# Kernel optimization log

Measured on AMD Instinct MI355X. Metric: run time of the kernel, lower is better.

## Reference

```python
import jax, jax.numpy as jnp
import numpy as np

D = 1024
H = 16
HD = D // H
EPS = 1e-5

def _ln(t, gamma, beta):
    # LayerNorm over last dim (head_dim)
    mu = jnp.mean(t, axis=-1, keepdims=True)
    var = jnp.mean(jnp.square(t - mu), axis=-1, keepdims=True)
    return (t - mu) * jax.lax.rsqrt(var + EPS) * gamma + beta

def setup_inputs() -> dict:
    key = jax.random.key(0)
    ks = jax.random.split(key, 6)
    B, S = 2, 2048
    # xavier_uniform bound for square [D,D] weight
    bound = float(np.sqrt(6.0 / (D + D)))
    x = jax.random.normal(ks[0], (B, S, D), dtype=jnp.float32)
    Wq = jax.random.uniform(ks[1], (D, D), jnp.float32, -bound, bound)
    Wk = jax.random.uniform(ks[2], (D, D), jnp.float32, -bound, bound)
    Wv = jax.random.uniform(ks[3], (D, D), jnp.float32, -bound, bound)
    Wp = jax.random.uniform(ks[4], (D, D), jnp.float32, -bound, bound)
    bp = jnp.zeros((D,), jnp.float32)
    gq = jnp.ones((HD,), jnp.float32); bq = jnp.zeros((HD,), jnp.float32)
    gk = jnp.ones((HD,), jnp.float32); bk = jnp.zeros((HD,), jnp.float32)
    return {"x": x, "Wq": Wq, "Wk": Wk, "Wv": Wv, "Wp": Wp, "bp": bp,
            "gq": gq, "bq": bq, "gk": gk, "bk": bk}

def reference(x, Wq, Wk, Wv, Wp, bp, gq, bq, gk, bk):
    B, S, _ = x.shape
    scale = HD ** -0.5
    # torch Linear: x @ W.T -> (B,S,H,HD) -> (B,H,S,HD)
    q = (x @ Wq.T).reshape(B, S, H, HD).transpose(0, 2, 1, 3)
    k = (x @ Wk.T).reshape(B, S, H, HD).transpose(0, 2, 1, 3)
    v = (x @ Wv.T).reshape(B, S, H, HD).transpose(0, 2, 1, 3)
    q = _ln(q, gq, bq)
    k = _ln(k, gk, bk)
    scores = jnp.einsum('bhqd,bhkd->bhqk', q, k) * scale
    causal_mask = jnp.triu(jnp.ones((S, S), dtype=bool), k=1)  # True above diagonal
    scores = jnp.where(causal_mask[None, None], -jnp.inf, scores)
    attn = jax.nn.softmax(scores, axis=-1)
    out = jnp.einsum('bhqk,bhkd->bhqd', attn, v).transpose(0, 2, 1, 3).reshape(B, S, D)
    out = out @ Wp.T + bp
    return (out, attn)
```

## Files before the change

### kernel.cpp

```cpp
#include <hip/hip_runtime.h>

typedef _Float16 f16;
typedef _Float16 f16x4 __attribute__((ext_vector_type(4)));
typedef _Float16 f16x8 __attribute__((ext_vector_type(8)));
typedef float f32x4 __attribute__((ext_vector_type(4)));

#define D_ 1024
#define H_ 16
#define HD_ 64
#define B_ 2
#define S_ 2048
#define M_ 4096
#define SCALE 0.125f
#define NEG_BIG -1e30f

__device__ __forceinline__ float red16_sum(float v) {
#pragma unroll
  for (int m = 8; m >= 1; m >>= 1) v += __shfl_xor(v, m);
  return v;
}

__device__ __forceinline__ void gload16(const f16* g, f16* l) {
  __builtin_amdgcn_global_load_lds((const __attribute__((address_space(1))) void*)g,
                                   (__attribute__((address_space(3))) void*)l, 16, 0, 0);
}

__global__ __launch_bounds__(256) void k_cvt5(const float* __restrict__ x,
    const float* __restrict__ w0, const float* __restrict__ w1,
    const float* __restrict__ w2, const float* __restrict__ w3,
    f16* __restrict__ xh, f16* __restrict__ wh)
{
  const int y = blockIdx.y;
  const float* src; f16* dst; int n4;
  if (y == 0) { src = x; dst = xh; n4 = (M_ * D_) / 4; }
  else {
    src = (y == 1) ? w0 : (y == 2) ? w1 : (y == 3) ? w2 : w3;
    dst = wh + (size_t)(y - 1) * D_ * D_;
    n4 = (D_ * D_) / 4;
  }
  const int stride = gridDim.x * blockDim.x;
  for (int i = blockIdx.x * blockDim.x + threadIdx.x; i < n4; i += stride) {
    f32x4 v = ((const f32x4*)src)[i];
    ((f16x4*)dst)[i] = (f16x4){(f16)v[0], (f16)v[1], (f16)v[2], (f16)v[3]};
  }
}

__device__ __forceinline__ void gemm128(const f16* __restrict__ A, const f16* __restrict__ Bw,
                                        int K, int bm, int bn, f32x4 acc[4][4])
{
  __shared__ f16 As[128][64];
  __shared__ f16 Bs[128][64];
  const int tid = threadIdx.x;
  const int lane = tid & 63, wid = tid >> 6;
  const int wr = wid >> 1, wc = wid & 1, g = lane >> 4, li = lane & 15;
  const int lrow = lane >> 3, lcol = (lane & 7) * 8;

#pragma unroll
  for (int m = 0; m < 4; ++m)
#pragma unroll
    for (int n = 0; n < 4; ++n)
      acc[m][n] = (f32x4){0.f, 0.f, 0.f, 0.f};

  for (int k0 = 0; k0 < K; k0 += 64) {
#pragma unroll
    for (int i = 0; i < 4; ++i) {
      int c = wid * 4 + i;
      int row = c * 8 + lrow;
      gload16(&A[(size_t)(bm + row) * K + k0 + lcol], &As[c * 8][0]);
      gload16(&Bw[(size_t)(bn + row) * K + k0 + lcol], &Bs[c * 8][0]);
    }
    __syncthreads();
#pragma unroll
    for (int kk = 0; kk < 64; kk += 32) {
      f16x8 af[4], bf[4];
#pragma unroll
      for (int m = 0; m < 4; ++m) af[m] = *(const f16x8*)&As[wr * 64 + m * 16 + li][kk + g * 8];
#pragma unroll
      for (int n = 0; n < 4; ++n) bf[n] = *(const f16x8*)&Bs[wc * 64 + n * 16 + li][kk + g * 8];
#pragma unroll
      for (int m = 0; m < 4; ++m)
#pragma unroll
        for (int n = 0; n < 4; ++n)
          acc[m][n] = __builtin_amdgcn_mfma_f32_16x16x32_f16(af[m], bf[n], acc[m][n], 0, 0, 0);
    }
    __syncthreads();
  }
}

__global__ __launch_bounds__(256) void k_gemm_qkv(const f16* __restrict__ xh,
    const f16* __restrict__ wh,
    const float* __restrict__ gq, const float* __restrict__ bq,
    const float* __restrict__ gk, const float* __restrict__ bk,
    f16* __restrict__ qt, f16* __restrict__ kt, f16* __restrict__ vh)
{
  const int z = blockIdx.z;
  const f16* Bw = wh + (size_t)z * D_ * D_;
  f16* C = (z == 0) ? qt : (z == 1) ? kt : vh;
  f32x4 acc[4][4];
  gemm128(xh, Bw, D_, blockIdx.x * 128, blockIdx.y * 128, acc);
  const int tid = threadIdx.x, lane = tid & 63, wid = tid >> 6;
  const int wr = wid >> 1, wc = wid & 1, g = lane >> 4, li = lane & 15;
  const int hh = blockIdx.y * 2 + wc;
  const float* gamma = (z == 0) ? gq : gk;
  const float* beta  = (z == 0) ? bq : bk;
  float gm[4], bt[4];
  if (z < 2) {
#pragma unroll
    for (int n = 0; n < 4; ++n) { gm[n] = gamma[n * 16 + li]; bt[n] = beta[n * 16 + li]; }
  }
#pragma unroll
  for (int m = 0; m < 4; ++m)
#pragma unroll
    for (int r = 0; r < 4; ++r) {
      int rr = blockIdx.x * 128 + wr * 64 + m * 16 + g * 4 + r;
      int b = rr >> 11, s = rr & (S_ - 1);
      float v0 = acc[m][0][r], v1 = acc[m][1][r], v2 = acc[m][2][r], v3 = acc[m][3][r];
      if (z < 2) {
        float mean = red16_sum(v0 + v1 + v2 + v3) * (1.f / 64.f);
        v0 -= mean; v1 -= mean; v2 -= mean; v3 -= mean;
        float ss = red16_sum(v0 * v0 + v1 * v1 + v2 * v2 + v3 * v3);
        float inv = rsqrtf(ss * (1.f / 64.f) + 1e-5f);
        v0 = v0 * inv * gm[0] + bt[0]; v1 = v1 * inv * gm[1] + bt[1];
        v2 = v2 * inv * gm[2] + bt[2]; v3 = v3 * inv * gm[3] + bt[3];
      }
      f16* dst = C + ((size_t)(b * H_ + hh) * S_ + s) * HD_;
      dst[li]      = (f16)v0;
      dst[16 + li] = (f16)v1;
      dst[32 + li] = (f16)v2;
      dst[48 + li] = (f16)v3;
    }
}

__global__ __launch_bounds__(256) void k_gemm_proj(const f16* __restrict__ oh,
    const f16* __restrict__ Wph, const float* __restrict__ bp, float* __restrict__ out)
{
  f32x4 acc[4][4];
  gemm128(oh, Wph, D_, blockIdx.x * 128, blockIdx.y * 128, acc);
  const int tid = threadIdx.x, lane = tid & 63, wid = tid >> 6;
  const int wr = wid >> 1, wc = wid & 1, g = lane >> 4, li = lane & 15;
#pragma unroll
  for (int m = 0; m < 4; ++m)
#pragma unroll
    for (int n = 0; n < 4; ++n)
#pragma unroll
      for (int r = 0; r < 4; ++r) {
        int rr = blockIdx.x * 128 + wr * 64 + m * 16 + g * 4 + r;
        int cc = blockIdx.y * 128 + wc * 64 + n * 16 + li;
        out[(size_t)rr * D_ + cc] = acc[m][n][r] + bp[cc];
      }
}

__global__ __launch_bounds__(256) void k_transpose_v(const f16* __restrict__ vh, f16* __restrict__ vt)
{
  __shared__ f16 T[64][72];
  const int tid = threadIdx.x;
  const int s0 = blockIdx.x * 64, h = blockIdx.y, b = blockIdx.z;
  const f16* src = vh + ((size_t)(b * H_ + h) * S_ + s0) * HD_;
#pragma unroll
  for (int i = 0; i < 2; ++i) {
    int slot = tid + i * 256, sl = slot >> 3, ch = (slot & 7) * 8;
    *(f16x8*)&T[sl][ch] = *(const f16x8*)&src[(size_t)sl * HD_ + ch];
  }
  __syncthreads();
#pragma unroll
  for (int i = 0; i < 2; ++i) {
    int slot = tid + i * 256, d = slot >> 3, sc = (slot & 7) * 8;
    f16x8 val;
#pragma unroll
    for (int j = 0; j < 8; ++j) val[j] = T[sc + j][d];
    *(f16x8*)&vt[((size_t)(b * H_ + h) * HD_ + d) * S_ + s0 + sc] = val;
  }
}

__global__ __launch_bounds__(256, 4) void k_attn_stats(const f16* __restrict__ qt,
    const f16* __restrict__ kt, float* __restrict__ lpart)
{
  __shared__ float Ls[2][64];
  const int tq = 31 - blockIdx.x;
  const int ks = blockIdx.y;
  const int bh = blockIdx.z;
  const int tid = threadIdx.x, lane = tid & 63, wid = tid >> 6;
  const int wr = wid >> 1, wc = wid & 1, g = lane >> 4, li = lane & 15;
  const int ntk = (tq + 2) >> 1;
  const int t0 = ks * 8, t1 = (ntk < (ks + 1) * 8) ? ntk : (ks + 1) * 8;
  float* lp = lpart + ((size_t)(bh * 32 + tq) * 2 + ks) * 64;
  if (t0 >= t1) { if (tid < 64) lp[tid] = 0.f; return; }

  const f16* Qb = qt + (size_t)bh * S_ * HD_;
  const f16* Kb = kt + (size_t)bh * S_ * HD_;

  f16x8 qa[2][2];
#pragma unroll
  for (int m = 0; m < 2; ++m)
#pragma unroll
    for (int kk = 0; kk < 2; ++kk)
      qa[m][kk] = *(const f16x8*)&Qb[(size_t)(tq * 64 + wr * 32 + m * 16 + li) * HD_ + kk * 32 + g * 8];

  float lrun[2][4];
#pragma unroll
  for (int m = 0; m < 2; ++m)
#pragma unroll
    for (int r = 0; r < 4; ++r) lrun[m][r] = 0.f;

  for (int tk = t0; tk < t1; ++tk) {
    f32x4 acc[2][4];
#pragma unroll
    for (int m = 0; m < 2; ++m)
#pragma unroll
      for (int n = 0; n < 4; ++n) acc[m][n] = (f32x4){0.f, 0.f, 0.f, 0.f};
#pragma unroll
    for (int kk = 0; kk < 2; ++kk) {
      f16x8 kf[4];
#pragma unroll
      for (int n = 0; n < 4; ++n)
        kf[n] = *(const f16x8*)&Kb[(size_t)(tk * 128 + wc * 64 + n * 16 + li) * HD_ + kk * 32 + g * 8];
#pragma unroll
      for (int m = 0; m < 2; ++m)
#pragma unroll
        for (int n = 0; n < 4; ++n)
          acc[m][n] = __builtin_amdgcn_mfma_f32_16x16x32_f16(qa[m][kk], kf[n], acc[m][n], 0, 0, 0);
    }
    const bool diag = (tk == ntk - 1);
#pragma unroll
    for (int m = 0; m < 2; ++m)
#pragma unroll
      for (int r = 0; r < 4; ++r) {
        int row = tq * 64 + wr * 32 + m * 16 + g * 4 + r;
#pragma unroll
        for (int n = 0; n < 4; ++n) {
          float sv = acc[m][n][r] * SCALE;
          if (diag) { int col = tk * 128 + wc * 64 + n * 16 + li; if (col > row) sv = NEG_BIG; }
          lrun[m][r] += __expf(sv);
        }
      }
  }

#pragma unroll
  for (int m = 0; m < 2; ++m)
#pragma unroll
    for (int r = 0; r < 4; ++r) lrun[m][r] = red16_sum(lrun[m][r]);

  if (li == 0) {
#pragma unroll
    for (int m = 0; m < 2; ++m)
#pragma unroll
      for (int r = 0; r < 4; ++r)
        Ls[wc][wr * 32 + m * 16 + g * 4 + r] = lrun[m][r];
  }
  __syncthreads();
  if (tid < 64) lp[tid] = Ls[0][tid] + Ls[1][tid];
}

__global__ __launch_bounds__(64, 4) void k_attn_fused(const f16* __restrict__ qt,
    const f16* __restrict__ kt, const f16* __restrict__ vt,
    const float* __restrict__ lpart, float* __restrict__ attn, f16* __restrict__ oh)
{
  __shared__ f16 Ps[16][138];
  const int bx = blockIdx.x;
  const int bh = bx & 31;
  const int s  = 127 - (bx >> 5);
  const int b = bh >> 4, h = bh & 15;
  const int lane = threadIdx.x;
  const int g = lane >> 4, li = lane & 15;
  const int row0 = s * 16;
  const int ntk = (s + 8) >> 3;
  const f16* Qb = qt + (size_t)bh * S_ * HD_;
  const f16* Kb = kt + (size_t)bh * S_ * HD_;
  float* attnB = attn + (size_t)bh * S_ * S_;
  const float* lp = lpart + (size_t)(bh * 32 + (s >> 2)) * 2 * 64;

  f16x8 qa[2];
#pragma unroll
  for (int kk = 0; kk < 2; ++kk)
    qa[kk] = *(const f16x8*)&Qb[(size_t)(row0 + li) * HD_ + kk * 32 + g * 8];

  float il[4];
#pragma unroll
  for (int r = 0; r < 4; ++r) {
    int lr = (s & 3) * 16 + g * 4 + r;
    il[r] = 1.f / (lp[lr] + lp[64 + lr]);
  }

  f32x4 oacc[4];
#pragma unroll
  for (int n = 0; n < 4; ++n) oacc[n] = (f32x4){0.f, 0.f, 0.f, 0.f};

  for (int tk = 0; tk < ntk; ++tk) {
    const bool diag = (tk == ntk - 1);
#pragma unroll
    for (int nh = 0; nh < 2; ++nh) {
      f32x4 acc[4];
#pragma unroll
      for (int j = 0; j < 4; ++j) acc[j] = (f32x4){0.f, 0.f, 0.f, 0.f};
#pragma unroll
      for (int kk = 0; kk < 2; ++kk) {
        f16x8 kf[4];
#pragma unroll
        for (int j = 0; j < 4; ++j)
          kf[j] = *(const f16x8*)&Kb[(size_t)(tk * 128 + nh * 64 + j * 16 + li) * HD_ + kk * 32 + g * 8];
#pragma unroll
        for (int j = 0; j < 4; ++j)
          acc[j] = __builtin_amdgcn_mfma_f32_16x16x32_f16(qa[kk], kf[j], acc[j], 0, 0, 0);
      }
#pragma unroll
      for (int r = 0; r < 4; ++r) {
        int row = row0 + g * 4 + r;
        float* rowp = attnB + (size_t)row * S_ + tk * 128 + nh * 64 + li;
#pragma unroll
        for (int j = 0; j < 4; ++j) {
          float sv = acc[j][r] * SCALE;
          if (diag) { int col = tk * 128 + nh * 64 + j * 16 + li; if (col > row) sv = NEG_BIG; }
          float p = __expf(sv) * il[r];
          __builtin_nontemporal_store(p, rowp + j * 16);
          Ps[g * 4 + r][nh * 64 + j * 16 + li] = (f16)p;
        }
      }
    }
#pragma unroll
    for (int kk = 0; kk < 4; ++kk) {
      f16x8 vbf[4];
#pragma unroll
      for (int n = 0; n < 4; ++n)
        vbf[n] = *(const f16x8*)&vt[((size_t)bh * HD_ + n * 16 + li) * S_ + tk * 128 + kk * 32 + g * 8];
      f16x8 pa = *(const f16x8*)&Ps[li][kk * 32 + g * 8];
#pragma unroll
      for (int n = 0; n < 4; ++n)
        oacc[n] = __builtin_amdgcn_mfma_f32_16x16x32_f16(pa, vbf[n], oacc[n], 0, 0, 0);
    }
  }

  {
    const int zr = lane >> 5, zc = (lane & 31) * 4;
    f32x4 z = {0.f, 0.f, 0.f, 0.f};
    for (int tk = ntk; tk < 16; ++tk) {
      float* a0 = attnB + (size_t)row0 * S_ + tk * 128;
#pragma unroll
      for (int rr = 0; rr < 16; rr += 2)
        __builtin_nontemporal_store(z, (f32x4*)(a0 + (size_t)(rr + zr) * S_ + zc));
    }
  }

#pragma unroll
  for (int n = 0; n < 4; ++n)
#pragma unroll
    for (int r = 0; r < 4; ++r)
      oh[(size_t)(b * S_ + row0 + g * 4 + r) * D_ + h * HD_ + n * 16 + li] = (f16)oacc[n][r];
}

extern "C" void kernel_launch(void* const* d_in, const int* in_sizes, int n_in,
                              void* d_out, int out_size, void* d_ws, size_t ws_size,
                              hipStream_t stream)
{
  (void)in_sizes; (void)n_in; (void)out_size; (void)ws_size;
  const float* x  = (const float*)d_in[0];
  const float* Wq = (const float*)d_in[1];
  const float* Wk = (const float*)d_in[2];
  const float* Wv = (const float*)d_in[3];
  const float* Wp = (const float*)d_in[4];
  const float* bp = (const float*)d_in[5];
  const float* gq = (const float*)d_in[6];
  const float* bq = (const float*)d_in[7];
  const float* gk = (const float*)d_in[8];
  const float* bk = (const float*)d_in[9];

  float* out  = (float*)d_out;
  float* attn = out + (size_t)B_ * S_ * D_;

  f16* xh  = (f16*)d_ws;
  f16* wh  = xh + (size_t)M_ * D_;
  f16* qt  = wh + (size_t)4 * D_ * D_;
  f16* kt  = qt + (size_t)M_ * D_;
  f16* vh  = kt + (size_t)M_ * D_;
  f16* vt  = vh + (size_t)M_ * D_;
  f16* oh  = vt + (size_t)M_ * D_;
  float* lpart = (float*)(oh + (size_t)M_ * D_);

  dim3 blk(256);
  k_cvt5<<<dim3(256, 5), blk, 0, stream>>>(x, Wq, Wk, Wv, Wp, xh, wh);
  k_gemm_qkv<<<dim3(32, 8, 3), blk, 0, stream>>>(xh, wh, gq, bq, gk, bk, qt, kt, vh);
  k_attn_stats<<<dim3(32, 2, 32), blk, 0, stream>>>(qt, kt, lpart);
  k_transpose_v<<<dim3(32, 16, 2), blk, 0, stream>>>(vh, vt);
  k_attn_fused<<<dim3(4096), dim3(64), 0, stream>>>(qt, kt, vt, lpart, attn, oh);
  k_gemm_proj<<<dim3(32, 8), blk, 0, stream>>>(oh, wh + (size_t)3 * D_ * D_, bp, out);
}
```

Before: 313.0 us.

## Fuse softmax row-sum pass into attention kernel, dropping separate stats kernel

Removes the separate k_attn_stats kernel and its lpart buffer. Each attention wavefront now runs its own first pass over K, computing QK^T and summing exp scores per row before the main normalized pass. This saves one kernel launch and the global round trip for the partial sums. In exchange, the 16-row wavefronts redo QK^T work that the stats kernel shared across 64-row tiles, with less K reuse and less parallelism for the row-sum pass.

```diff
diff --git a/kernel.cpp b/kernel.cpp
--- a/kernel.cpp
+++ b/kernel.cpp
@@ -172,88 +172,9 @@
   }
 }
 
-__global__ __launch_bounds__(256, 4) void k_attn_stats(const f16* __restrict__ qt,
-    const f16* __restrict__ kt, float* __restrict__ lpart)
-{
-  __shared__ float Ls[2][64];
-  const int tq = 31 - blockIdx.x;
-  const int ks = blockIdx.y;
-  const int bh = blockIdx.z;
-  const int tid = threadIdx.x, lane = tid & 63, wid = tid >> 6;
-  const int wr = wid >> 1, wc = wid & 1, g = lane >> 4, li = lane & 15;
-  const int ntk = (tq + 2) >> 1;
-  const int t0 = ks * 8, t1 = (ntk < (ks + 1) * 8) ? ntk : (ks + 1) * 8;
-  float* lp = lpart + ((size_t)(bh * 32 + tq) * 2 + ks) * 64;
-  if (t0 >= t1) { if (tid < 64) lp[tid] = 0.f; return; }
-
-  const f16* Qb = qt + (size_t)bh * S_ * HD_;
-  const f16* Kb = kt + (size_t)bh * S_ * HD_;
-
-  f16x8 qa[2][2];
-#pragma unroll
-  for (int m = 0; m < 2; ++m)
-#pragma unroll
-    for (int kk = 0; kk < 2; ++kk)
-      qa[m][kk] = *(const f16x8*)&Qb[(size_t)(tq * 64 + wr * 32 + m * 16 + li) * HD_ + kk * 32 + g * 8];
-
-  float lrun[2][4];
-#pragma unroll
-  for (int m = 0; m < 2; ++m)
-#pragma unroll
-    for (int r = 0; r < 4; ++r) lrun[m][r] = 0.f;
-
-  for (int tk = t0; tk < t1; ++tk) {
-    f32x4 acc[2][4];
-#pragma unroll
-    for (int m = 0; m < 2; ++m)
-#pragma unroll
-      for (int n = 0; n < 4; ++n) acc[m][n] = (f32x4){0.f, 0.f, 0.f, 0.f};
-#pragma unroll
-    for (int kk = 0; kk < 2; ++kk) {
-      f16x8 kf[4];
-#pragma unroll
-      for (int n = 0; n < 4; ++n)
-        kf[n] = *(const f16x8*)&Kb[(size_t)(tk * 128 + wc * 64 + n * 16 + li) * HD_ + kk * 32 + g * 8];
-#pragma unroll
-      for (int m = 0; m < 2; ++m)
-#pragma unroll
-        for (int n = 0; n < 4; ++n)
-          acc[m][n] = __builtin_amdgcn_mfma_f32_16x16x32_f16(qa[m][kk], kf[n], acc[m][n], 0, 0, 0);
-    }
-    const bool diag = (tk == ntk - 1);
-#pragma unroll
-    for (int m = 0; m < 2; ++m)
-#pragma unroll
-      for (int r = 0; r < 4; ++r) {
-        int row = tq * 64 + wr * 32 + m * 16 + g * 4 + r;
-#pragma unroll
-        for (int n = 0; n < 4; ++n) {
-          float sv = acc[m][n][r] * SCALE;
-          if (diag) { int col = tk * 128 + wc * 64 + n * 16 + li; if (col > row) sv = NEG_BIG; }
-          lrun[m][r] += __expf(sv);
-        }
-      }
-  }
-
-#pragma unroll
-  for (int m = 0; m < 2; ++m)
-#pragma unroll
-    for (int r = 0; r < 4; ++r) lrun[m][r] = red16_sum(lrun[m][r]);
-
-  if (li == 0) {
-#pragma unroll
-    for (int m = 0; m < 2; ++m)
-#pragma unroll
-      for (int r = 0; r < 4; ++r)
-        Ls[wc][wr * 32 + m * 16 + g * 4 + r] = lrun[m][r];
-  }
-  __syncthreads();
-  if (tid < 64) lp[tid] = Ls[0][tid] + Ls[1][tid];
-}
-
 __global__ __launch_bounds__(64, 4) void k_attn_fused(const f16* __restrict__ qt,
     const f16* __restrict__ kt, const f16* __restrict__ vt,
-    const float* __restrict__ lpart, float* __restrict__ attn, f16* __restrict__ oh)
+    float* __restrict__ attn, f16* __restrict__ oh)
 {
   __shared__ f16 Ps[16][138];
   const int bx = blockIdx.x;
@@ -267,19 +188,48 @@
   const f16* Qb = qt + (size_t)bh * S_ * HD_;
   const f16* Kb = kt + (size_t)bh * S_ * HD_;
   float* attnB = attn + (size_t)bh * S_ * S_;
-  const float* lp = lpart + (size_t)(bh * 32 + (s >> 2)) * 2 * 64;
 
   f16x8 qa[2];
 #pragma unroll
   for (int kk = 0; kk < 2; ++kk)
     qa[kk] = *(const f16x8*)&Qb[(size_t)(row0 + li) * HD_ + kk * 32 + g * 8];
 
+  float lrun[4];
+#pragma unroll
+  for (int r = 0; r < 4; ++r) lrun[r] = 0.f;
+
+  for (int tk = 0; tk < ntk; ++tk) {
+    const bool diag = (tk == ntk - 1);
+#pragma unroll
+    for (int nh = 0; nh < 2; ++nh) {
+      f32x4 acc[4];
+#pragma unroll
+      for (int j = 0; j < 4; ++j) acc[j] = (f32x4){0.f, 0.f, 0.f, 0.f};
+#pragma unroll
+      for (int kk = 0; kk < 2; ++kk) {
+        f16x8 kf[4];
+#pragma unroll
+        for (int j = 0; j < 4; ++j)
+          kf[j] = *(const f16x8*)&Kb[(size_t)(tk * 128 + nh * 64 + j * 16 + li) * HD_ + kk * 32 + g * 8];
+#pragma unroll
+        for (int j = 0; j < 4; ++j)
+          acc[j] = __builtin_amdgcn_mfma_f32_16x16x32_f16(qa[kk], kf[j], acc[j], 0, 0, 0);
+      }
+#pragma unroll
+      for (int r = 0; r < 4; ++r) {
+        int row = row0 + g * 4 + r;
+#pragma unroll
+        for (int j = 0; j < 4; ++j) {
+          float sv = acc[j][r] * SCALE;
+          if (diag) { int col = tk * 128 + nh * 64 + j * 16 + li; if (col > row) sv = NEG_BIG; }
+          lrun[r] += __expf(sv);
+        }
+      }
+    }
+  }
   float il[4];
 #pragma unroll
-  for (int r = 0; r < 4; ++r) {
-    int lr = (s & 3) * 16 + g * 4 + r;
-    il[r] = 1.f / (lp[lr] + lp[64 + lr]);
-  }
+  for (int r = 0; r < 4; ++r) il[r] = 1.f / red16_sum(lrun[r]);
 
   f32x4 oacc[4];
 #pragma unroll
@@ -373,13 +323,11 @@
   f16* vh  = kt + (size_t)M_ * D_;
   f16* vt  = vh + (size_t)M_ * D_;
   f16* oh  = vt + (size_t)M_ * D_;
-  float* lpart = (float*)(oh + (size_t)M_ * D_);
 
   dim3 blk(256);
   k_cvt5<<<dim3(256, 5), blk, 0, stream>>>(x, Wq, Wk, Wv, Wp, xh, wh);
   k_gemm_qkv<<<dim3(32, 8, 3), blk, 0, stream>>>(xh, wh, gq, bq, gk, bk, qt, kt, vh);
-  k_attn_stats<<<dim3(32, 2, 32), blk, 0, stream>>>(qt, kt, lpart);
   k_transpose_v<<<dim3(32, 16, 2), blk, 0, stream>>>(vh, vt);
-  k_attn_fused<<<dim3(4096), dim3(64), 0, stream>>>(qt, kt, vt, lpart, attn, oh);
+  k_attn_fused<<<dim3(4096), dim3(64), 0, stream>>>(qt, kt, vt, attn, oh);
   k_gemm_proj<<<dim3(32, 8), blk, 0, stream>>>(oh, wh + (size_t)3 * D_ * D_, bp, out);
 }
```

Result: no change. 314.2 us (+0.4%).
